# Kernel optimization log

Hardware: AMD Instinct MI355X
Metric: run time of the kernel (lower is better)

The kernel has to match this reference:

```python
import jax, jax.numpy as jnp
from jax import lax
import numpy as np

MAX_BLOCK = 8   # max_block_size
LOOP = 1000     # loop
C, H, W = 3, 4096, 4096


def local_pixel_shuffle(image, key):
    """Faithful JAX version of LocalPixelShuffling.__call__ (prob branch taken).

    Each of LOOP iterations samples per-spatial-dim window sizes ws in
    [1, MAX_BLOCK] and positions, then for every channel shuffles the window
    contents *taken from the original image* and writes them into the running
    output (later windows overwrite earlier ones), exactly as the torch code.
    Implemented jit-compatibly with fixed-size (MAX_BLOCK x MAX_BLOCK) patches
    plus a mask for the true window.
    """
    M = MAX_BLOCK * MAX_BLOCK
    orig = image
    r = jnp.arange(MAX_BLOCK)
    # sort keys >= 2.0 keep non-window elements after all rand values in [0,1)
    big = jnp.arange(M, dtype=jnp.float32) + 2.0

    def step(temp, k):
        kh, kw, kph, kpw, kperm = jax.random.split(k, 5)
        # window sizes: randint inclusive [1, MAX_BLOCK] like random.randint
        wsh = jax.random.randint(kh, (), 1, MAX_BLOCK + 1)
        wsw = jax.random.randint(kw, (), 1, MAX_BLOCK + 1)
        # window positions uniform in [0, dim - ws]
        ph = (jax.random.uniform(kph) * (H - wsh + 1).astype(jnp.float32)).astype(jnp.int32)
        pw = (jax.random.uniform(kpw) * (W - wsw + 1).astype(jnp.float32)).astype(jnp.int32)
        # fixed-size patch start (clamped so the static slice stays in bounds)
        psh = jnp.clip(ph, 0, H - MAX_BLOCK)
        psw = jnp.clip(pw, 0, W - MAX_BLOCK)
        offh = ph - psh
        offw = pw - psw
        mask = (((r >= offh) & (r < offh + wsh))[:, None]
                & ((r >= offw) & (r < offw + wsw))[None, :]).reshape(M)

        patch = lax.dynamic_slice(orig, (0, psh, psw), (C, MAX_BLOCK, MAX_BLOCK)).reshape(C, M)
        # independent permutation per channel, restricted to in-window elements
        rand = jax.random.uniform(kperm, (C, M))
        sortkey = jnp.where(mask[None, :], rand, big[None, :])
        order = jnp.argsort(sortkey, axis=1)          # masked elems in random order, then unmasked in index order
        tpos = jnp.argsort(~mask)                     # masked positions first (stable)
        inv = jnp.argsort(tpos)
        vals = jnp.take_along_axis(patch, order, axis=1)
        shuffled = vals[:, inv]                       # shuffled[:, p] = correct value for flat position p

        cur = lax.dynamic_slice(temp, (0, psh, psw), (C, MAX_BLOCK, MAX_BLOCK)).reshape(C, M)
        write = jnp.where(mask[None, :], shuffled, cur).reshape(C, MAX_BLOCK, MAX_BLOCK)
        temp = lax.dynamic_update_slice(temp, write, (0, psh, psw))
        return temp, None

    keys = jax.random.split(key, LOOP)
    out, _ = lax.scan(step, image, keys)
    return out


def setup_inputs() -> dict:
    key = jax.random.key(0)
    image = jax.random.normal(key, (C, H, W), dtype=jnp.float32)
    return {"image": image, "seed": 0}


def reference(image, seed):
    key = jax.random.key(seed)
    return local_pixel_shuffle(image, key)
```

## Files before the change

### kernel.cpp

```cpp
#include <hip/hip_runtime.h>
#include <stdint.h>

#define HH 4096
#define WW 4096
#define CC 3
#define NLOOP 1000
#define NCOPY 8192
#define NTHR 256
#define N4 ((CC * HH * WW) / 4)
#define CSTRIDE (NCOPY * NTHR)
static_assert(N4 == 6 * CSTRIDE, "copy loop must be exactly 6 iterations");

typedef float vfloat4 __attribute__((ext_vector_type(4)));

struct Rec {
  int psh, psw;
  unsigned long long live;
  float vals[CC][64];
};
static_assert(sizeof(Rec) == 784, "rec size");

__device__ __forceinline__ void tf2x32(uint32_t k0, uint32_t k1,
                                       uint32_t x0, uint32_t x1,
                                       uint32_t& o0, uint32_t& o1) {
  const uint32_t ks2 = k0 ^ k1 ^ 0x1BD11BDAu;
  x0 += k0; x1 += k1;
#define ROTL_(v,r) (((v)<<(r))|((v)>>(32-(r))))
#define RND_(r) { x0 += x1; x1 = ROTL_(x1,(r)); x1 ^= x0; }
  RND_(13) RND_(15) RND_(26) RND_(6)
  x0 += k1; x1 += ks2 + 1u;
  RND_(17) RND_(29) RND_(16) RND_(24)
  x0 += ks2; x1 += k0 + 2u;
  RND_(13) RND_(15) RND_(26) RND_(6)
  x0 += k0; x1 += k1 + 3u;
  RND_(17) RND_(29) RND_(16) RND_(24)
  x0 += k1; x1 += ks2 + 4u;
  RND_(13) RND_(15) RND_(26) RND_(6)
  x0 += ks2; x1 += k0 + 5u;
  o0 = x0; o1 = x1;
#undef RND_
#undef ROTL_
}

__device__ __forceinline__ uint32_t rb32(uint32_t k0, uint32_t k1,
                                         uint32_t x0, uint32_t x1) {
  uint32_t o0, o1;
  tf2x32(k0, k1, x0, x1, o0, o1);
  return o0 ^ o1;
}

__device__ __forceinline__ void geom(uint32_t K1, int j,
                                     int& ph, int& pw, int& wsh, int& wsw) {
  uint32_t k0, k1, a0, a1;
  tf2x32(0u, K1, 0u, (uint32_t)j, k0, k1);
  uint32_t kh0,kh1,kw0,kw1,kp0,kp1,kq0,kq1;
  tf2x32(k0,k1,0u,0u,kh0,kh1);
  tf2x32(k0,k1,0u,1u,kw0,kw1);
  tf2x32(k0,k1,0u,2u,kp0,kp1);
  tf2x32(k0,k1,0u,3u,kq0,kq1);
  tf2x32(kh0,kh1,0u,1u,a0,a1);
  wsh = 1 + (int)(rb32(a0,a1,0u,0u) & 7u);
  tf2x32(kw0,kw1,0u,1u,a0,a1);
  wsw = 1 + (int)(rb32(a0,a1,0u,0u) & 7u);
  const float uh = __uint_as_float(0x3F800000u | (rb32(kp0,kp1,0u,0u) >> 9)) - 1.0f;
  const float uw = __uint_as_float(0x3F800000u | (rb32(kq0,kq1,0u,0u) >> 9)) - 1.0f;
  ph = (int)(uh * (float)(HH - wsh + 1));
  pw = (int)(uw * (float)(WW - wsw + 1));
}

__global__ __launch_bounds__(NTHR) void k_main(
    const int* __restrict__ seedp, Rec* __restrict__ rec,
    const float* __restrict__ in, float* __restrict__ out) {
  const int b = blockIdx.x;
  const int tid = threadIdx.x;
  if (b >= NLOOP) {
    const vfloat4* __restrict__ in4 = (const vfloat4*)in;
    vfloat4* __restrict__ out4 = (vfloat4*)out;
    int idx = (b - NLOOP) * NTHR + tid;
    #pragma unroll
    for (int k = 0; k < 6; ++k) {
      const int i = idx + k * CSTRIDE;
      vfloat4 v = in4[i];
      __builtin_nontemporal_store(v, &out4[i]);
    }
    return;
  }

  const int i = b;
  const uint32_t K1 = (uint32_t)seedp[0];

  __shared__ uint32_t rb[CC * 64];
  __shared__ unsigned char mlist[64];
  __shared__ unsigned char srcbuf[CC][64];
  __shared__ unsigned long long shred[NTHR];

  int ph, pw, wsh, wsw;
  geom(K1, i, ph, pw, wsh, wsw);
  const int psh = min(ph, HH - 8);
  const int psw = min(pw, WW - 8);
  const int offh = ph - psh, offw = pw - psw;
  const uint32_t colm = ((1u << wsw) - 1u) << offw;
  unsigned long long rows = (wsh == 8) ? ~0ull : ((1ull << (8 * wsh)) - 1ull);
  rows <<= (8 * offh);
  const unsigned long long mask =
      rows & (0x0101010101010101ull * (unsigned long long)colm);

  {
    uint32_t k0, k1, kr0, kr1;
    tf2x32(0u, K1, 0u, (uint32_t)i, k0, k1);
    tf2x32(k0, k1, 0u, 4u, kr0, kr1);
    if (tid < CC * 64) rb[tid] = rb32(kr0, kr1, 0u, (uint32_t)tid) >> 9;
  }

  unsigned long long clr = 0ull;
  for (int j = i + 1 + tid; j < NLOOP; j += NTHR) {
    int phj, pwj, whj, wwj;
    geom(K1, j, phj, pwj, whj, wwj);
    const int r0 = max(0, phj - psh), r1 = min(8, phj + whj - psh);
    const int c0 = max(0, pwj - psw), c1 = min(8, pwj + wwj - psw);
    if (r0 < r1 && c0 < c1) {
      const uint32_t cm = ((1u << (c1 - c0)) - 1u) << c0;
      const int nr = r1 - r0;
      unsigned long long rr = (nr == 8) ? ~0ull : ((1ull << (8 * nr)) - 1ull);
      rr <<= (8 * r0);
      clr |= rr & (0x0101010101010101ull * (unsigned long long)cm);
    }
  }
  shred[tid] = clr;

  if (tid < 64) {
    srcbuf[0][tid] = (unsigned char)tid;
    srcbuf[1][tid] = (unsigned char)tid;
    srcbuf[2][tid] = (unsigned char)tid;
    const int ordinal =
        __popcll(mask & ((tid == 0) ? 0ull : ((1ull << tid) - 1ull)));
    if ((mask >> tid) & 1ull) mlist[ordinal] = (unsigned char)tid;
  }
  __syncthreads();

  for (int s = NTHR / 2; s > 0; s >>= 1) {
    if (tid < s) shred[tid] |= shred[tid + s];
    __syncthreads();
  }
  const unsigned long long live = mask & ~shred[0];

  if (tid < CC * 64) {
    const int c = tid >> 6, q = tid & 63;
    if ((mask >> q) & 1ull) {
      const uint32_t myk = rb[(c << 6) | q];
      int rank = 0;
      for (int q2 = 0; q2 < 64; ++q2) {
        if ((mask >> q2) & 1ull) {
          const uint32_t k2 = rb[(c << 6) | q2];
          if (k2 < myk || (k2 == myk && q2 < q)) ++rank;
        }
      }
      srcbuf[c][mlist[rank]] = (unsigned char)q;
    }
  }
  __syncthreads();

  if (tid < CC * 64) {
    const int c = tid >> 6, q = tid & 63;
    float v = 0.0f;
    if ((live >> q) & 1ull) {
      const int s = srcbuf[c][q];
      const size_t base = (size_t)c * (size_t)HH * (size_t)WW;
      v = in[base + (size_t)(psh + (s >> 3)) * WW + (size_t)(psw + (s & 7))];
    }
    rec[i].vals[c][q] = v;
  }
  if (tid == 0) {
    rec[i].psh = psh; rec[i].psw = psw; rec[i].live = live;
  }
}

__global__ __launch_bounds__(192) void k_scatter(
    const Rec* __restrict__ rec, float* __restrict__ out) {
  const int i = blockIdx.x;
  const int t = threadIdx.x;
  const int c = t >> 6, q = t & 63;
  const unsigned long long live = rec[i].live;
  if ((live >> q) & 1ull) {
    const int psh = rec[i].psh, psw = rec[i].psw;
    const size_t base = (size_t)c * (size_t)HH * (size_t)WW;
    out[base + (size_t)(psh + (q >> 3)) * WW + (size_t)(psw + (q & 7))] =
        rec[i].vals[c][q];
  }
}

extern "C" void kernel_launch(void* const* d_in, const int* in_sizes, int n_in,
                              void* d_out, int out_size, void* d_ws, size_t ws_size,
                              hipStream_t stream) {
  const float* img = (const float*)d_in[0];
  const int* seed = (const int*)d_in[1];
  float* out = (float*)d_out;
  Rec* rec = (Rec*)d_ws;

  hipLaunchKernelGGL(k_main, dim3(NLOOP + NCOPY), dim3(NTHR), 0, stream,
                     seed, rec, img, out);
  hipLaunchKernelGGL(k_scatter, dim3(NLOOP), dim3(192), 0, stream, rec, out);
}
```

Baseline: 79.10 us.

## Precompute window geometry once and move overwrite-mask computation to the scatter kernel

The first kernel now computes each iteration's geometry once and stores it in a small int4 table, along with a compact descriptor of source indices. It no longer recomputes the geometry of every later window with Threefry hashes inside each block. The second kernel reads the table to find which pixels later windows overwrite and gathers directly from the input image. This replaces roughly O(N^2) hash work in the first kernel with cheap table reads in the second, at the cost of a larger second kernel that performs the gather. Copy blocks are also placed ahead of descriptor blocks in the grid.

```diff
diff --git a/kernel.cpp b/kernel.cpp
--- a/kernel.cpp
+++ b/kernel.cpp
@@ -13,12 +13,13 @@
 
 typedef float vfloat4 __attribute__((ext_vector_type(4)));
 
-struct Rec {
+struct Desc {
   int psh, psw;
-  unsigned long long live;
-  float vals[CC][64];
+  unsigned long long mask;
+  unsigned char src[CC][64];
+  unsigned char pad[48];
 };
-static_assert(sizeof(Rec) == 784, "rec size");
+static_assert(sizeof(Desc) == 256, "desc size");
 
 __device__ __forceinline__ void tf2x32(uint32_t k0, uint32_t k1,
                                        uint32_t x0, uint32_t x1,
@@ -49,34 +50,15 @@
   return o0 ^ o1;
 }
 
-__device__ __forceinline__ void geom(uint32_t K1, int j,
-                                     int& ph, int& pw, int& wsh, int& wsw) {
-  uint32_t k0, k1, a0, a1;
-  tf2x32(0u, K1, 0u, (uint32_t)j, k0, k1);
-  uint32_t kh0,kh1,kw0,kw1,kp0,kp1,kq0,kq1;
-  tf2x32(k0,k1,0u,0u,kh0,kh1);
-  tf2x32(k0,k1,0u,1u,kw0,kw1);
-  tf2x32(k0,k1,0u,2u,kp0,kp1);
-  tf2x32(k0,k1,0u,3u,kq0,kq1);
-  tf2x32(kh0,kh1,0u,1u,a0,a1);
-  wsh = 1 + (int)(rb32(a0,a1,0u,0u) & 7u);
-  tf2x32(kw0,kw1,0u,1u,a0,a1);
-  wsw = 1 + (int)(rb32(a0,a1,0u,0u) & 7u);
-  const float uh = __uint_as_float(0x3F800000u | (rb32(kp0,kp1,0u,0u) >> 9)) - 1.0f;
-  const float uw = __uint_as_float(0x3F800000u | (rb32(kq0,kq1,0u,0u) >> 9)) - 1.0f;
-  ph = (int)(uh * (float)(HH - wsh + 1));
-  pw = (int)(uw * (float)(WW - wsw + 1));
-}
-
-__global__ __launch_bounds__(NTHR) void k_main(
-    const int* __restrict__ seedp, Rec* __restrict__ rec,
+__global__ __launch_bounds__(NTHR) void k_copy_desc(
+    const int* __restrict__ seedp, Desc* __restrict__ d, int4* __restrict__ geo,
     const float* __restrict__ in, float* __restrict__ out) {
   const int b = blockIdx.x;
   const int tid = threadIdx.x;
-  if (b >= NLOOP) {
+  if (b < NCOPY) {
     const vfloat4* __restrict__ in4 = (const vfloat4*)in;
     vfloat4* __restrict__ out4 = (vfloat4*)out;
-    int idx = (b - NLOOP) * NTHR + tid;
+    const int idx = b * NTHR + tid;
     #pragma unroll
     for (int k = 0; k < 6; ++k) {
       const int i = idx + k * CSTRIDE;
@@ -86,47 +68,45 @@
     return;
   }
 
-  const int i = b;
+  const int i = b - NCOPY;
   const uint32_t K1 = (uint32_t)seedp[0];
 
   __shared__ uint32_t rb[CC * 64];
   __shared__ unsigned char mlist[64];
   __shared__ unsigned char srcbuf[CC][64];
-  __shared__ unsigned long long shred[NTHR];
 
-  int ph, pw, wsh, wsw;
-  geom(K1, i, ph, pw, wsh, wsw);
+  uint32_t k0, k1, a0, a1;
+  tf2x32(0u, K1, 0u, (uint32_t)i, k0, k1);
+
+  uint32_t kh0,kh1,kw0,kw1,kp0,kp1,kq0,kq1,kr0,kr1;
+  tf2x32(k0,k1,0u,0u,kh0,kh1);
+  tf2x32(k0,k1,0u,1u,kw0,kw1);
+  tf2x32(k0,k1,0u,2u,kp0,kp1);
+  tf2x32(k0,k1,0u,3u,kq0,kq1);
+  tf2x32(k0,k1,0u,4u,kr0,kr1);
+
+  if (tid < CC * 64) rb[tid] = rb32(kr0, kr1, 0u, (uint32_t)tid) >> 9;
+
+  tf2x32(kh0,kh1,0u,1u,a0,a1);
+  const int wsh = 1 + (int)(rb32(a0,a1,0u,0u) & 7u);
+  tf2x32(kw0,kw1,0u,1u,a0,a1);
+  const int wsw = 1 + (int)(rb32(a0,a1,0u,0u) & 7u);
+
+  const float uh = __uint_as_float(0x3F800000u | (rb32(kp0,kp1,0u,0u) >> 9)) - 1.0f;
+  const float uw = __uint_as_float(0x3F800000u | (rb32(kq0,kq1,0u,0u) >> 9)) - 1.0f;
+
+  const int ph = (int)(uh * (float)(HH - wsh + 1));
+  const int pw = (int)(uw * (float)(WW - wsw + 1));
   const int psh = min(ph, HH - 8);
   const int psw = min(pw, WW - 8);
-  const int offh = ph - psh, offw = pw - psw;
+  const int offh = ph - psh;
+  const int offw = pw - psw;
+
   const uint32_t colm = ((1u << wsw) - 1u) << offw;
   unsigned long long rows = (wsh == 8) ? ~0ull : ((1ull << (8 * wsh)) - 1ull);
   rows <<= (8 * offh);
   const unsigned long long mask =
       rows & (0x0101010101010101ull * (unsigned long long)colm);
-
-  {
-    uint32_t k0, k1, kr0, kr1;
-    tf2x32(0u, K1, 0u, (uint32_t)i, k0, k1);
-    tf2x32(k0, k1, 0u, 4u, kr0, kr1);
-    if (tid < CC * 64) rb[tid] = rb32(kr0, kr1, 0u, (uint32_t)tid) >> 9;
-  }
-
-  unsigned long long clr = 0ull;
-  for (int j = i + 1 + tid; j < NLOOP; j += NTHR) {
-    int phj, pwj, whj, wwj;
-    geom(K1, j, phj, pwj, whj, wwj);
-    const int r0 = max(0, phj - psh), r1 = min(8, phj + whj - psh);
-    const int c0 = max(0, pwj - psw), c1 = min(8, pwj + wwj - psw);
-    if (r0 < r1 && c0 < c1) {
-      const uint32_t cm = ((1u << (c1 - c0)) - 1u) << c0;
-      const int nr = r1 - r0;
-      unsigned long long rr = (nr == 8) ? ~0ull : ((1ull << (8 * nr)) - 1ull);
-      rr <<= (8 * r0);
-      clr |= rr & (0x0101010101010101ull * (unsigned long long)cm);
-    }
-  }
-  shred[tid] = clr;
 
   if (tid < 64) {
     srcbuf[0][tid] = (unsigned char)tid;
@@ -136,13 +116,8 @@
         __popcll(mask & ((tid == 0) ? 0ull : ((1ull << tid) - 1ull)));
     if ((mask >> tid) & 1ull) mlist[ordinal] = (unsigned char)tid;
   }
+  if (tid == 0) geo[i] = make_int4(ph, pw, wsh, wsw);
   __syncthreads();
-
-  for (int s = NTHR / 2; s > 0; s >>= 1) {
-    if (tid < s) shred[tid] |= shred[tid + s];
-    __syncthreads();
-  }
-  const unsigned long long live = mask & ~shred[0];
 
   if (tid < CC * 64) {
     const int c = tid >> 6, q = tid & 63;
@@ -162,30 +137,49 @@
 
   if (tid < CC * 64) {
     const int c = tid >> 6, q = tid & 63;
-    float v = 0.0f;
-    if ((live >> q) & 1ull) {
-      const int s = srcbuf[c][q];
-      const size_t base = (size_t)c * (size_t)HH * (size_t)WW;
-      v = in[base + (size_t)(psh + (s >> 3)) * WW + (size_t)(psw + (s & 7))];
-    }
-    rec[i].vals[c][q] = v;
+    d[i].src[c][q] = srcbuf[c][q];
   }
   if (tid == 0) {
-    rec[i].psh = psh; rec[i].psw = psw; rec[i].live = live;
+    d[i].psh = psh; d[i].psw = psw; d[i].mask = mask;
   }
 }
 
-__global__ __launch_bounds__(192) void k_scatter(
-    const Rec* __restrict__ rec, float* __restrict__ out) {
+__global__ __launch_bounds__(NTHR) void k_live_apply(
+    const float* __restrict__ in, float* __restrict__ out,
+    const Desc* __restrict__ d, const int4* __restrict__ geo) {
   const int i = blockIdx.x;
   const int t = threadIdx.x;
-  const int c = t >> 6, q = t & 63;
-  const unsigned long long live = rec[i].live;
-  if ((live >> q) & 1ull) {
-    const int psh = rec[i].psh, psw = rec[i].psw;
-    const size_t base = (size_t)c * (size_t)HH * (size_t)WW;
-    out[base + (size_t)(psh + (q >> 3)) * WW + (size_t)(psw + (q & 7))] =
-        rec[i].vals[c][q];
+  const int psh = d[i].psh, psw = d[i].psw;
+  unsigned long long clr = 0ull;
+  for (int j = i + 1 + t; j < NLOOP; j += NTHR) {
+    const int4 g = geo[j];
+    const int r0 = max(0, g.x - psh), r1 = min(8, g.x + g.z - psh);
+    const int c0 = max(0, g.y - psw), c1 = min(8, g.y + g.w - psw);
+    if (r0 < r1 && c0 < c1) {
+      const uint32_t cm = ((1u << (c1 - c0)) - 1u) << c0;
+      const int nr = r1 - r0;
+      unsigned long long rr = (nr == 8) ? ~0ull : ((1ull << (8 * nr)) - 1ull);
+      rr <<= (8 * r0);
+      clr |= rr & (0x0101010101010101ull * (unsigned long long)cm);
+    }
+  }
+  __shared__ unsigned long long sh[NTHR];
+  sh[t] = clr;
+  __syncthreads();
+  for (int s = NTHR / 2; s > 0; s >>= 1) {
+    if (t < s) sh[t] |= sh[t + s];
+    __syncthreads();
+  }
+  const unsigned long long live = d[i].mask & ~sh[0];
+
+  if (t < CC * 64) {
+    const int c = t >> 6, q = t & 63;
+    if ((live >> q) & 1ull) {
+      const int s = d[i].src[c][q];
+      const size_t base = (size_t)c * (size_t)HH * (size_t)WW;
+      out[base + (size_t)(psh + (q >> 3)) * WW + (size_t)(psw + (q & 7))] =
+          in[base + (size_t)(psh + (s >> 3)) * WW + (size_t)(psw + (s & 7))];
+    }
   }
 }
 
@@ -195,9 +189,11 @@
   const float* img = (const float*)d_in[0];
   const int* seed = (const int*)d_in[1];
   float* out = (float*)d_out;
-  Rec* rec = (Rec*)d_ws;
+  Desc* d = (Desc*)d_ws;
+  int4* geo = (int4*)((char*)d_ws + NLOOP * sizeof(Desc));
 
-  hipLaunchKernelGGL(k_main, dim3(NLOOP + NCOPY), dim3(NTHR), 0, stream,
-                     seed, rec, img, out);
-  hipLaunchKernelGGL(k_scatter, dim3(NLOOP), dim3(192), 0, stream, rec, out);
+  hipLaunchKernelGGL(k_copy_desc, dim3(NCOPY + NLOOP), dim3(NTHR), 0, stream,
+                     seed, d, geo, img, out);
+  hipLaunchKernelGGL(k_live_apply, dim3(NLOOP), dim3(NTHR), 0, stream,
+                     img, out, d, geo);
 }
```

Result: faster. 76.19 us (-3.7%).
